# Kernel optimization log

Hardware: AMD Instinct MI355X
Metric: run time of the kernel (lower is better)

The kernel has to match this reference:

```python
import jax, jax.numpy as jnp
import numpy as np

DN = ('NHWC', 'HWIO', 'NHWC')


def setup_inputs() -> dict:
    key = jax.random.key(0)
    ks = jax.random.split(key, 5)
    B, H, W, C = 2, 256, 256, 192
    heads = 4
    x = jax.random.normal(ks[0], (B, H, W, C), dtype=jnp.float32)
    w_qkv = jax.random.normal(ks[1], (1, 1, C, 3 * C), dtype=jnp.float32) * 0.05
    b_qkv = jnp.zeros((3 * C,), dtype=jnp.float32)
    w_dw = jax.random.normal(ks[2], (3, 3, 1, 3 * C), dtype=jnp.float32) * 0.05
    b_dw = jnp.zeros((3 * C,), dtype=jnp.float32)
    temperature = jnp.ones((1, heads, 1, 1), dtype=jnp.float32)
    w_out = jax.random.normal(ks[3], (1, 1, C, C), dtype=jnp.float32) * 0.05
    b_out = jnp.zeros((C,), dtype=jnp.float32)
    return {"x": x, "w_qkv": w_qkv, "b_qkv": b_qkv, "w_dw": w_dw,
            "b_dw": b_dw, "temperature": temperature, "w_out": w_out,
            "b_out": b_out}


def _mdta(x, w_qkv, b_qkv, w_dw, b_dw, temperature, w_out, b_out):
    B, H, W, C = x.shape
    heads = temperature.shape[1]
    c = C // heads  # per-head channels
    # 1x1 pointwise qkv projection -> [B,H,W,3C]
    qkv = jax.lax.conv_general_dilated(x, w_qkv, (1, 1), 'SAME',
                                       dimension_numbers=DN) + b_qkv
    # 3x3 depthwise conv (groups = 3C)
    qkv = jax.lax.conv_general_dilated(qkv, w_dw, (1, 1), 'SAME',
                                       dimension_numbers=DN,
                                       feature_group_count=3 * C) + b_dw
    q, k, v = jnp.split(qkv, 3, axis=-1)  # each [B,H,W,C]

    def to_heads(t):
        # [B,H,W,C] -> [B, heads, c, HW]
        return t.reshape(B, H * W, heads, c).transpose(0, 2, 3, 1)

    q, k, v = to_heads(q), to_heads(k), to_heads(v)
    # L2-normalize along the spatial (HW) axis
    q = q / jnp.maximum(jnp.linalg.norm(q, axis=-1, keepdims=True), 1e-12)
    k = k / jnp.maximum(jnp.linalg.norm(k, axis=-1, keepdims=True), 1e-12)
    # channel-wise transposed attention: [B,heads,c,c]
    attn = jnp.einsum('bhcn,bhdn->bhcd', q, k) * temperature
    attn = jax.nn.softmax(attn, axis=-1)
    out = jnp.einsum('bhcd,bhdn->bhcn', attn, v)  # [B,heads,c,HW]
    out = out.transpose(0, 3, 1, 2).reshape(B, H, W, C)
    # output 1x1 projection
    out = jax.lax.conv_general_dilated(out, w_out, (1, 1), 'SAME',
                                       dimension_numbers=DN) + b_out
    return out


def reference(x, w_qkv, b_qkv, w_dw, b_dw, temperature, w_out, b_out):
    return _mdta(x, w_qkv, b_qkv, w_dw, b_dw, temperature, w_out, b_out)
```

## Files before the change

kernel.cpp:

```cpp
#include <hip/hip_runtime.h>

typedef unsigned short ushort_t;
typedef __attribute__((ext_vector_type(8))) short short8;
typedef __attribute__((ext_vector_type(4))) float f32x4;

#define B_ 2
#define HW_ 65536
#define MTOT_ 131072
#define C_ 192
#define C3_ 576
#define HEADS_ 4
#define CH_ 48

#define OFF_QKV0  ((size_t)0)
#define OFF_QKV1  ((size_t)150994944)
#define OFF_XB    OFF_QKV1
#define OFF_BT    ((size_t)301989888)
#define OFF_S     ((size_t)302211072)
#define OFF_NQ    ((size_t)302284800)
#define OFF_NK    ((size_t)302286336)
#define OFF_ATTN  ((size_t)302287872)
#define OFF_MT    ((size_t)302361600)

__device__ __forceinline__ float b2f(ushort_t u) {
    unsigned v = ((unsigned)u) << 16;
    return __builtin_bit_cast(float, v);
}
__device__ __forceinline__ ushort_t f2b(float f) {
    unsigned u = __builtin_bit_cast(unsigned, f);
    u = (u + 0x7fffu + ((u >> 16) & 1u)) >> 16;
    return (ushort_t)u;
}
__device__ __forceinline__ void storev(float* p, float v) { *p = v; }
__device__ __forceinline__ void storev(ushort_t* p, float v) { *p = f2b(v); }

__global__ void k_cvt_x(const float* __restrict__ x, ushort_t* __restrict__ xb) {
    int i = (blockIdx.x * 256 + threadIdx.x) * 8;
    float4 a = *(const float4*)(x + i);
    float4 b = *(const float4*)(x + i + 4);
    ushort_t o[8];
    o[0] = f2b(a.x); o[1] = f2b(a.y); o[2] = f2b(a.z); o[3] = f2b(a.w);
    o[4] = f2b(b.x); o[5] = f2b(b.y); o[6] = f2b(b.z); o[7] = f2b(b.w);
    *(uint4*)(xb + i) = *(uint4*)o;
}

__global__ void k0_transpose(const float* __restrict__ w, ushort_t* __restrict__ bt) {
    int idx = blockIdx.x * 256 + threadIdx.x;
    int n = idx / 192, k = idx - n * 192;
    bt[idx] = f2b(w[k * 576 + n]);
}

template <typename OutT>
__global__ __launch_bounds__(256) void gemm_k192(
    const ushort_t* __restrict__ A, int lda, int acol0,
    const ushort_t* __restrict__ BT, int bstride,
    const float* __restrict__ bias,
    OutT* __restrict__ Cout, int ldc)
{
    const int m0 = blockIdx.y * 64;
    const int n0 = blockIdx.x * 64;
    const ushort_t* bt = BT + (bstride ? (size_t)(m0 >> 16) * (size_t)bstride : 0);

    __shared__ ushort_t As[64 * 72];
    __shared__ ushort_t Bs[64 * 72];

    const int t = threadIdx.x;
    const int wave = t >> 6, lane = t & 63;
    const int quad = lane >> 4, l15 = lane & 15;
    const int wm = (wave >> 1) * 32, wn = (wave & 1) * 32;
    const int srow = t >> 2, scol = (t & 3) * 16;

    f32x4 acc[2][2] = {};

    for (int kk = 0; kk < 192; kk += 64) {
        const ushort_t* ga = A + (size_t)(m0 + srow) * lda + acol0 + kk + scol;
        uint4 va0 = *(const uint4*)ga;
        uint4 va1 = *(const uint4*)(ga + 8);
        const ushort_t* gb = bt + (size_t)(n0 + srow) * 192 + kk + scol;
        uint4 vb0 = *(const uint4*)gb;
        uint4 vb1 = *(const uint4*)(gb + 8);
        *(uint4*)&As[srow * 72 + scol] = va0;
        *(uint4*)&As[srow * 72 + scol + 8] = va1;
        *(uint4*)&Bs[srow * 72 + scol] = vb0;
        *(uint4*)&Bs[srow * 72 + scol + 8] = vb1;
        __syncthreads();
#pragma unroll
        for (int ks = 0; ks < 2; ks++) {
            short8 a0 = *(const short8*)&As[(wm + l15) * 72 + ks * 32 + quad * 8];
            short8 a1 = *(const short8*)&As[(wm + 16 + l15) * 72 + ks * 32 + quad * 8];
            short8 b0 = *(const short8*)&Bs[(wn + l15) * 72 + ks * 32 + quad * 8];
            short8 b1 = *(const short8*)&Bs[(wn + 16 + l15) * 72 + ks * 32 + quad * 8];
            acc[0][0] = __builtin_amdgcn_mfma_f32_16x16x32_bf16(a0, b0, acc[0][0], 0, 0, 0);
            acc[0][1] = __builtin_amdgcn_mfma_f32_16x16x32_bf16(a0, b1, acc[0][1], 0, 0, 0);
            acc[1][0] = __builtin_amdgcn_mfma_f32_16x16x32_bf16(a1, b0, acc[1][0], 0, 0, 0);
            acc[1][1] = __builtin_amdgcn_mfma_f32_16x16x32_bf16(a1, b1, acc[1][1], 0, 0, 0);
        }
        __syncthreads();
    }
#pragma unroll
    for (int sm = 0; sm < 2; sm++) {
#pragma unroll
        for (int sn = 0; sn < 2; sn++) {
            int col = n0 + wn + sn * 16 + l15;
            float bv = bias ? bias[col] : 0.f;
#pragma unroll
            for (int r = 0; r < 4; r++) {
                int row = m0 + wm + sm * 16 + quad * 4 + r;
                storev(&Cout[(size_t)row * ldc + col], acc[sm][sn][r] + bv);
            }
        }
    }
}

#define R_STRIP 16

__global__ __launch_bounds__(256) void k2_dwconv(const ushort_t* __restrict__ qkv0,
        const float* __restrict__ wdw, const float* __restrict__ bdw,
        ushort_t* __restrict__ qkv1)
{
    const int tid = blockIdx.x * 256 + threadIdx.x;
    const int c8 = tid % 72;
    const int t1 = tid / 72;
    const int x  = t1 & 255;
    const int t2 = t1 >> 8;
    const int s  = t2 & 15;
    const int b  = t2 >> 4;
    const int y0 = s * R_STRIP;
    const int cbase = c8 * 8;

    const bool xm = (x > 0), xp = (x < 255);
    const ushort_t* colbase = qkv0 + ((size_t)(b * HW_ + x) * C3_ + cbase);
    ushort_t*       ocol    = qkv1 + ((size_t)(b * HW_ + x) * C3_ + cbase);
    const size_t rstride = (size_t)256 * C3_;

    float w[3][3][8], bw[8];
#pragma unroll
    for (int ky = 0; ky < 3; ++ky)
#pragma unroll
        for (int kx = 0; kx < 3; ++kx) {
            const float* wp = wdw + ((ky * 3 + kx) * C3_ + cbase);
            float4 lo = *(const float4*)wp;
            float4 hi = *(const float4*)(wp + 4);
            w[ky][kx][0] = lo.x; w[ky][kx][1] = lo.y; w[ky][kx][2] = lo.z; w[ky][kx][3] = lo.w;
            w[ky][kx][4] = hi.x; w[ky][kx][5] = hi.y; w[ky][kx][6] = hi.z; w[ky][kx][7] = hi.w;
        }
    {
        float4 lo = *(const float4*)(bdw + cbase);
        float4 hi = *(const float4*)(bdw + cbase + 4);
        bw[0] = lo.x; bw[1] = lo.y; bw[2] = lo.z; bw[3] = lo.w;
        bw[4] = hi.x; bw[5] = hi.y; bw[6] = hi.z; bw[7] = hi.w;
    }

    const uint4 z4 = make_uint4(0, 0, 0, 0);
    auto loadrow = [&](int r, uint4& d0, uint4& d1, uint4& d2) {
        if ((unsigned)r <= 255u) {
            const ushort_t* p = colbase + (size_t)r * rstride;
            d1 = *(const uint4*)p;
            d0 = xm ? *(const uint4*)(p - C3_) : z4;
            d2 = xp ? *(const uint4*)(p + C3_) : z4;
        } else { d0 = z4; d1 = z4; d2 = z4; }
    };

    float A[3][8] = {};
    uint4 c0, c1, c2;
    loadrow(y0 - 1, c0, c1, c2);

#pragma unroll
    for (int RR = 0; RR < R_STRIP + 2; ++RR) {
        const int r = y0 - 1 + RR;
        uint4 n0 = z4, n1 = z4, n2 = z4;
        if (RR < R_STRIP + 1) loadrow(r + 1, n0, n1, n2);

        float rf[3][8];
        {
            const ushort_t* dd = (const ushort_t*)&c0;
#pragma unroll
            for (int j = 0; j < 8; ++j) rf[0][j] = b2f(dd[j]);
            dd = (const ushort_t*)&c1;
#pragma unroll
            for (int j = 0; j < 8; ++j) rf[1][j] = b2f(dd[j]);
            dd = (const ushort_t*)&c2;
#pragma unroll
            for (int j = 0; j < 8; ++j) rf[2][j] = b2f(dd[j]);
        }

        if (RR >= 1 && RR <= R_STRIP) {
#pragma unroll
            for (int kx = 0; kx < 3; ++kx)
#pragma unroll
                for (int j = 0; j < 8; ++j)
                    A[RR % 3][j] = fmaf(rf[kx][j], w[1][kx][j], A[RR % 3][j]);
        }
        if (RR <= R_STRIP - 1) {
#pragma unroll
            for (int kx = 0; kx < 3; ++kx)
#pragma unroll
                for (int j = 0; j < 8; ++j)
                    A[(RR + 1) % 3][j] = fmaf(rf[kx][j], w[0][kx][j], A[(RR + 1) % 3][j]);
        }
        if (RR >= 2) {
#pragma unroll
            for (int kx = 0; kx < 3; ++kx)
#pragma unroll
                for (int j = 0; j < 8; ++j)
                    A[(RR + 2) % 3][j] = fmaf(rf[kx][j], w[2][kx][j], A[(RR + 2) % 3][j]);
            ushort_t ov[8];
#pragma unroll
            for (int j = 0; j < 8; ++j) {
                ov[j] = f2b(A[(RR + 2) % 3][j] + bw[j]);
                A[(RR + 2) % 3][j] = 0.f;
            }
            *(uint4*)(ocol + (size_t)(r - 1) * rstride) = *(uint4*)ov;
        }
        c0 = n0; c1 = n1; c2 = n2;
    }
}

__global__ __launch_bounds__(256) void k3_gram(const ushort_t* __restrict__ qkv1,
        float* __restrict__ S, float* __restrict__ NQ, float* __restrict__ NK)
{
    int bh = blockIdx.y;
    int b = bh >> 2, h = bh & 3;
    int n0 = blockIdx.x * 512;
    __shared__ float Lq[32][49];
    __shared__ float Lk[32][49];
    int t = threadIdx.x;
    int cq0 = (t >> 4) * 3, ck0 = (t & 15) * 3;
    float acc[3][3] = {};
    float nacc = 0.f;

    for (int c0 = 0; c0 < 512; c0 += 32) {
        for (int i = t; i < 384; i += 256) {
            int row = i / 12, s = i - row * 12;
            int ch = (s < 6) ? (h * CH_ + s * 8) : (C_ + h * CH_ + (s - 6) * 8);
            uint4 d = *(const uint4*)(qkv1 + ((size_t)(b * HW_ + n0 + c0 + row)) * C3_ + ch);
            const ushort_t* dd = (const ushort_t*)&d;
            float* dst = (s < 6) ? &Lq[row][s * 8] : &Lk[row][(s - 6) * 8];
#pragma unroll
            for (int j = 0; j < 8; j++) dst[j] = b2f(dd[j]);
        }
        __syncthreads();
#pragma unroll 4
        for (int n = 0; n < 32; n++) {
            float q0 = Lq[n][cq0], q1 = Lq[n][cq0 + 1], q2 = Lq[n][cq0 + 2];
            float k0 = Lk[n][ck0], k1 = Lk[n][ck0 + 1], k2 = Lk[n][ck0 + 2];
            acc[0][0] += q0 * k0; acc[0][1] += q0 * k1; acc[0][2] += q0 * k2;
            acc[1][0] += q1 * k0; acc[1][1] += q1 * k1; acc[1][2] += q1 * k2;
            acc[2][0] += q2 * k0; acc[2][1] += q2 * k1; acc[2][2] += q2 * k2;
            if (t < 96) { float v = (t < 48) ? Lq[n][t] : Lk[n][t - 48]; nacc += v * v; }
        }
        __syncthreads();
    }
    float* Sp = S + bh * 2304;
#pragma unroll
    for (int i = 0; i < 3; i++)
#pragma unroll
        for (int j = 0; j < 3; j++)
            atomicAdd(&Sp[(cq0 + i) * 48 + ck0 + j], acc[i][j]);
    if (t < 48) atomicAdd(&NQ[bh * 48 + t], nacc);
    else if (t < 96) atomicAdd(&NK[bh * 48 + t - 48], nacc);
}

__global__ void k4a_softmax(const float* __restrict__ S, const float* __restrict__ NQ,
                            const float* __restrict__ NK, const float* __restrict__ temp,
                            float* __restrict__ ATT)
{
    int bh = blockIdx.y, cq = blockIdx.x;
    int h = bh & 3;
    int t = threadIdx.x;
    float nq = fmaxf(sqrtf(NQ[bh * 48 + cq]), 1e-12f);
    float tv = temp[h];
    float logit = -1e30f;
    if (t < 48) {
        float nk = fmaxf(sqrtf(NK[bh * 48 + t]), 1e-12f);
        logit = S[bh * 2304 + cq * 48 + t] * tv / (nq * nk);
    }
    float m = logit;
    for (int o = 32; o > 0; o >>= 1) m = fmaxf(m, __shfl_xor(m, o));
    float e = (t < 48) ? __expf(logit - m) : 0.f;
    float ssum = e;
    for (int o = 32; o > 0; o >>= 1) ssum += __shfl_xor(ssum, o);
    if (t < 48) ATT[bh * 2304 + cq * 48 + t] = e / ssum;
}

__global__ void k4b_buildM(const float* __restrict__ ATT, const float* __restrict__ wout,
                           ushort_t* __restrict__ MT)
{
    int idx = blockIdx.x * 256 + threadIdx.x;
    int b = idx / 36864; int rem = idx - b * 36864;
    int j = rem / 192;   int d = rem - j * 192;
    int h = d / 48, dd = d - h * 48;
    const float* ap = ATT + (size_t)(b * 4 + h) * 2304 + dd;
    const float* wp = wout + (size_t)(h * 48) * 192 + j;
    float s = 0.f;
#pragma unroll 8
    for (int cq = 0; cq < 48; cq++) s += ap[cq * 48] * wp[cq * 192];
    MT[idx] = f2b(s);
}

extern "C" void kernel_launch(void* const* d_in, const int* in_sizes, int n_in,
                              void* d_out, int out_size, void* d_ws, size_t ws_size,
                              hipStream_t stream) {
    const float* x     = (const float*)d_in[0];
    const float* w_qkv = (const float*)d_in[1];
    const float* b_qkv = (const float*)d_in[2];
    const float* w_dw  = (const float*)d_in[3];
    const float* b_dw  = (const float*)d_in[4];
    const float* temp  = (const float*)d_in[5];
    const float* w_out = (const float*)d_in[6];
    const float* b_out = (const float*)d_in[7];
    float* out = (float*)d_out;

    char* ws = (char*)d_ws;
    ushort_t* qkv0 = (ushort_t*)(ws + OFF_QKV0);
    ushort_t* qkv1 = (ushort_t*)(ws + OFF_QKV1);
    ushort_t* xb   = (ushort_t*)(ws + OFF_XB);
    ushort_t* btq  = (ushort_t*)(ws + OFF_BT);
    float*    Sb   = (float*)(ws + OFF_S);
    float*    NQ   = (float*)(ws + OFF_NQ);
    float*    NK   = (float*)(ws + OFF_NK);
    float*    ATT  = (float*)(ws + OFF_ATTN);
    ushort_t* MT   = (ushort_t*)(ws + OFF_MT);

    hipMemsetAsync(ws + OFF_S, 0, 76800, stream);

    k_cvt_x<<<12288, 256, 0, stream>>>(x, xb);
    k0_transpose<<<432, 256, 0, stream>>>(w_qkv, btq);
    gemm_k192<ushort_t><<<dim3(9, 2048), 256, 0, stream>>>(xb, 192, 0, btq, 0, b_qkv, qkv0, 576);
    k2_dwconv<<<2304, 256, 0, stream>>>(qkv0, w_dw, b_dw, qkv1);
    k3_gram<<<dim3(128, 8), 256, 0, stream>>>(qkv1, Sb, NQ, NK);
    k4a_softmax<<<dim3(48, 8), 64, 0, stream>>>(Sb, NQ, NK, temp, ATT);
    k4b_buildM<<<288, 256, 0, stream>>>(ATT, w_out, MT);
    gemm_k192<float><<<dim3(3, 2048), 256, 0, stream>>>(qkv1, 576, 384, MT, 36864, b_out, out, 192);
}
```

Measured before the change: 507.6 us.

## Compute Gram matrix and norms with bf16 MFMA and a deterministic two-stage reduction

```diff
diff --git a/kernel.cpp b/kernel.cpp
--- a/kernel.cpp
+++ b/kernel.cpp
@@ -15,6 +15,7 @@
 #define OFF_QKV0  ((size_t)0)
 #define OFF_QKV1  ((size_t)150994944)
 #define OFF_XB    OFF_QKV1
+#define OFF_P     OFF_QKV0
 #define OFF_BT    ((size_t)301989888)
 #define OFF_S     ((size_t)302211072)
 #define OFF_NQ    ((size_t)302284800)
@@ -216,49 +217,107 @@
     }
 }
 
-__global__ __launch_bounds__(256) void k3_gram(const ushort_t* __restrict__ qkv1,
+#define GR_LDSSTRIDE 136
+
+__global__ __launch_bounds__(256) void k3_gram_mfma(const ushort_t* __restrict__ qkv1,
+        float* __restrict__ P)
+{
+    const int bh = blockIdx.y;
+    const int b = bh >> 2, h = bh & 3;
+    const int slice = blockIdx.x;
+    const int t = threadIdx.x;
+    const int wave = t >> 6, lane = t & 63;
+    const int quad = lane >> 4, l15 = lane & 15;
+
+    __shared__ float red[7680];
+    ushort_t* Z = (ushort_t*)red;
+
+    f32x4 acc[15] = {};
+    const ushort_t* basep = qkv1 + (size_t)(b * HW_) * C3_;
+    const int row = t & 127;
+    const int seghalf = t >> 7;
+
+    for (int tile = 0; tile < 8; ++tile) {
+        const int nbase = slice * 1024 + tile * 128;
+        uint4 u[6];
+#pragma unroll
+        for (int k = 0; k < 6; ++k) {
+            int seg = k * 2 + seghalf;
+            int cg = (seg < 6) ? (h * CH_ + seg * 8) : (C_ + h * CH_ + (seg - 6) * 8);
+            u[k] = *(const uint4*)(basep + (size_t)(nbase + row) * C3_ + cg);
+        }
+        __syncthreads();
+#pragma unroll
+        for (int k = 0; k < 6; ++k) {
+            int seg = k * 2 + seghalf;
+            int zc = seg * 8;
+            const ushort_t* dd = (const ushort_t*)&u[k];
+#pragma unroll
+            for (int j = 0; j < 8; ++j)
+                Z[(zc + j) * GR_LDSSTRIDE + row] = dd[j];
+        }
+        __syncthreads();
+        const int n0 = wave * 32 + quad * 8;
+        short8 F[6];
+#pragma unroll
+        for (int c = 0; c < 6; ++c)
+            F[c] = *(const short8*)&Z[(c * 16 + l15) * GR_LDSSTRIDE + n0];
+#pragma unroll
+        for (int i = 0; i < 3; ++i)
+#pragma unroll
+            for (int j = 0; j < 3; ++j)
+                acc[i * 3 + j] = __builtin_amdgcn_mfma_f32_16x16x32_bf16(F[i], F[3 + j], acc[i * 3 + j], 0, 0, 0);
+#pragma unroll
+        for (int i = 0; i < 3; ++i) {
+            acc[9 + i]  = __builtin_amdgcn_mfma_f32_16x16x32_bf16(F[i], F[i], acc[9 + i], 0, 0, 0);
+            acc[12 + i] = __builtin_amdgcn_mfma_f32_16x16x32_bf16(F[3 + i], F[3 + i], acc[12 + i], 0, 0, 0);
+        }
+    }
+
+    __syncthreads();
+    if (wave & 1) {
+        float* dst = red + (wave >> 1) * (15 * 256);
+#pragma unroll
+        for (int tt = 0; tt < 15; ++tt)
+            *(f32x4*)&dst[tt * 256 + lane * 4] = acc[tt];
+    }
+    __syncthreads();
+    if (!(wave & 1)) {
+        const float* src = red + (wave >> 1) * (15 * 256);
+        const int sp = slice * 2 + (wave >> 1);
+#pragma unroll
+        for (int tt = 0; tt < 15; ++tt) {
+            f32x4 v = *(const f32x4*)&src[tt * 256 + lane * 4];
+#pragma unroll
+            for (int r = 0; r < 4; ++r) {
+                int e = (quad * 4 + r) * 16 + l15;
+                P[(((size_t)bh * 15 + tt) * 128 + sp) * 256 + e] = acc[tt][r] + v[r];
+            }
+        }
+    }
+}
+
+__global__ __launch_bounds__(256) void k3r_reduce(const float* __restrict__ P,
         float* __restrict__ S, float* __restrict__ NQ, float* __restrict__ NK)
 {
-    int bh = blockIdx.y;
-    int b = bh >> 2, h = bh & 3;
-    int n0 = blockIdx.x * 512;
-    __shared__ float Lq[32][49];
-    __shared__ float Lk[32][49];
-    int t = threadIdx.x;
-    int cq0 = (t >> 4) * 3, ck0 = (t & 15) * 3;
-    float acc[3][3] = {};
-    float nacc = 0.f;
-
-    for (int c0 = 0; c0 < 512; c0 += 32) {
-        for (int i = t; i < 384; i += 256) {
-            int row = i / 12, s = i - row * 12;
-            int ch = (s < 6) ? (h * CH_ + s * 8) : (C_ + h * CH_ + (s - 6) * 8);
-            uint4 d = *(const uint4*)(qkv1 + ((size_t)(b * HW_ + n0 + c0 + row)) * C3_ + ch);
-            const ushort_t* dd = (const ushort_t*)&d;
-            float* dst = (s < 6) ? &Lq[row][s * 8] : &Lk[row][(s - 6) * 8];
-#pragma unroll
-            for (int j = 0; j < 8; j++) dst[j] = b2f(dd[j]);
-        }
-        __syncthreads();
-#pragma unroll 4
-        for (int n = 0; n < 32; n++) {
-            float q0 = Lq[n][cq0], q1 = Lq[n][cq0 + 1], q2 = Lq[n][cq0 + 2];
-            float k0 = Lk[n][ck0], k1 = Lk[n][ck0 + 1], k2 = Lk[n][ck0 + 2];
-            acc[0][0] += q0 * k0; acc[0][1] += q0 * k1; acc[0][2] += q0 * k2;
-            acc[1][0] += q1 * k0; acc[1][1] += q1 * k1; acc[1][2] += q1 * k2;
-            acc[2][0] += q2 * k0; acc[2][1] += q2 * k1; acc[2][2] += q2 * k2;
-            if (t < 96) { float v = (t < 48) ? Lq[n][t] : Lk[n][t - 48]; nacc += v * v; }
-        }
-        __syncthreads();
-    }
-    float* Sp = S + bh * 2304;
-#pragma unroll
-    for (int i = 0; i < 3; i++)
-#pragma unroll
-        for (int j = 0; j < 3; j++)
-            atomicAdd(&Sp[(cq0 + i) * 48 + ck0 + j], acc[i][j]);
-    if (t < 48) atomicAdd(&NQ[bh * 48 + t], nacc);
-    else if (t < 96) atomicAdd(&NK[bh * 48 + t - 48], nacc);
+    int idx = blockIdx.x * 256 + threadIdx.x;
+    int bh = idx / 3840;
+    int rem = idx - bh * 3840;
+    int tt = rem >> 8;
+    int e = rem & 255;
+    const float* p = P + (((size_t)bh * 15 + tt) * 128) * 256 + e;
+    float s = 0.f;
+#pragma unroll 8
+    for (int sp = 0; sp < 128; ++sp) s += p[(size_t)sp * 256];
+    int r = e >> 4, c = e & 15;
+    if (tt < 9) {
+        int i = tt / 3, j = tt - i * 3;
+        S[bh * 2304 + (i * 16 + r) * 48 + j * 16 + c] = s;
+    } else if (tt < 12) {
+        if (r == c) NQ[bh * 48 + (tt - 9) * 16 + r] = s;
+    } else {
+        if (r == c) NK[bh * 48 + (tt - 12) * 16 + r] = s;
+    }
 }
 
 __global__ void k4a_softmax(const float* __restrict__ S, const float* __restrict__ NQ,
@@ -315,6 +374,7 @@
     ushort_t* qkv0 = (ushort_t*)(ws + OFF_QKV0);
     ushort_t* qkv1 = (ushort_t*)(ws + OFF_QKV1);
     ushort_t* xb   = (ushort_t*)(ws + OFF_XB);
+    float*    Pb   = (float*)(ws + OFF_P);
     ushort_t* btq  = (ushort_t*)(ws + OFF_BT);
     float*    Sb   = (float*)(ws + OFF_S);
     float*    NQ   = (float*)(ws + OFF_NQ);
@@ -322,13 +382,12 @@
     float*    ATT  = (float*)(ws + OFF_ATTN);
     ushort_t* MT   = (ushort_t*)(ws + OFF_MT);
 
-    hipMemsetAsync(ws + OFF_S, 0, 76800, stream);
-
     k_cvt_x<<<12288, 256, 0, stream>>>(x, xb);
     k0_transpose<<<432, 256, 0, stream>>>(w_qkv, btq);
     gemm_k192<ushort_t><<<dim3(9, 2048), 256, 0, stream>>>(xb, 192, 0, btq, 0, b_qkv, qkv0, 576);
     k2_dwconv<<<2304, 256, 0, stream>>>(qkv0, w_dw, b_dw, qkv1);
-    k3_gram<<<dim3(128, 8), 256, 0, stream>>>(qkv1, Sb, NQ, NK);
+    k3_gram_mfma<<<dim3(64, 8), 256, 0, stream>>>(qkv1, Pb);
+    k3r_reduce<<<120, 256, 0, stream>>>(Pb, Sb, NQ, NK);
     k4a_softmax<<<dim3(48, 8), 64, 0, stream>>>(Sb, NQ, NK, temp, ATT);
     k4b_buildM<<<288, 256, 0, stream>>>(ATT, w_out, MT);
     gemm_k192<float><<<dim3(3, 2048), 256, 0, stream>>>(qkv1, 576, 384, MT, 36864, b_out, out, 192);
```

New measurement: 449.1 us. 1.13x faster.
